# Performance work log

Hardware: AMD Instinct MI355X
Metric: run time of the kernel (lower is better)

## Reference

```python
import jax, jax.numpy as jnp
import numpy as np

DIM = 1280
HEADS = 16
HD = DIM // HEADS  # 80
NSEG = 8
LSEG = 1024
SEQ = NSEG * LSEG  # 8192


def _rotate_half(x):
    x1, x2 = jnp.split(x, 2, axis=-1)
    return jnp.concatenate([-x2, x1], axis=-1)


def setup_inputs() -> dict:
    key = jax.random.key(0)
    ks = jax.random.split(key, 6)
    hidden_states = jax.random.normal(ks[0], (SEQ, DIM), dtype=jnp.float32)
    # rotary embedding table: per-position angles over head_dim
    inv_freq = 1.0 / (10000.0 ** (np.arange(0, HD, 2, dtype=np.float32) / HD))
    pos = np.arange(SEQ, dtype=np.float32)
    freqs = np.outer(pos, inv_freq)                    # [SEQ, HD/2]
    emb = np.concatenate([freqs, freqs], axis=-1)      # [SEQ, HD]
    cos = jnp.asarray(np.cos(emb), dtype=jnp.float32)
    sin = jnp.asarray(np.sin(emb), dtype=jnp.float32)
    w_scale = 1.0 / np.sqrt(DIM)
    qkv_w = jax.random.normal(ks[1], (DIM, 3 * DIM), dtype=jnp.float32) * w_scale
    qkv_b = jax.random.normal(ks[2], (3 * DIM,), dtype=jnp.float32) * 0.02
    proj_w = jax.random.normal(ks[3], (DIM, DIM), dtype=jnp.float32) * w_scale
    proj_b = jax.random.normal(ks[4], (DIM,), dtype=jnp.float32) * 0.02
    cu_seqlens = jnp.arange(NSEG + 1, dtype=jnp.int32) * LSEG
    return {
        "hidden_states": hidden_states,
        "cos": cos,
        "sin": sin,
        "qkv_w": qkv_w,
        "qkv_b": qkv_b,
        "proj_w": proj_w,
        "proj_b": proj_b,
        "cu_seqlens": cu_seqlens,
    }


def reference(hidden_states, cos, sin, qkv_w, qkv_b, proj_w, proj_b, cu_seqlens):
    S, D = hidden_states.shape
    n_seg = cu_seqlens.shape[0] - 1          # static
    L = S // n_seg                            # equal-length packed segments
    # fused QKV projection: [S, 3D] -> q, k, v each [S, H, hd]
    qkv = hidden_states @ qkv_w + qkv_b
    q, k, v = (t.reshape(S, HEADS, HD) for t in jnp.split(qkv, 3, axis=-1))
    # RoPE (computed in fp32, as in apply_rotary_pos_emb_vision)
    c = cos.astype(jnp.float32)[:, None, :]   # [S, 1, hd]
    s = sin.astype(jnp.float32)[:, None, :]
    qf = q.astype(jnp.float32)
    kf = k.astype(jnp.float32)
    q = (qf * c + _rotate_half(qf) * s).astype(q.dtype)
    k = (kf * c + _rotate_half(kf) * s).astype(k.dtype)
    # block-diagonal varlen attention == independent attention per segment
    qs = q.reshape(n_seg, L, HEADS, HD)
    ks = k.reshape(n_seg, L, HEADS, HD)
    vs = v.reshape(n_seg, L, HEADS, HD)
    scale = HD ** -0.5
    scores = jnp.einsum("nqhd,nkhd->nhqk", qs, ks) * scale
    probs = jax.nn.softmax(scores.astype(jnp.float32), axis=-1).astype(qs.dtype)
    out = jnp.einsum("nhqk,nkhd->nqhd", probs, vs)     # [n, L, H, hd]
    out = out.reshape(S, D)
    return out @ proj_w + proj_b
```

## Files before the change

### kernel.cpp

```cpp
#include <hip/hip_runtime.h>

#define SEQ   8192
#define DIM   1280
#define HEADS 16
#define HD    80
#define LSEG  1024
#define QKVD  3840

typedef unsigned short USHORT;
typedef __attribute__((ext_vector_type(8))) short bf16x8;
typedef __attribute__((ext_vector_type(4))) float f32x4;
typedef __attribute__((ext_vector_type(4))) USHORT u16x4;
typedef __attribute__((ext_vector_type(4))) int i32x4;

#define CSF  0.16129832f
#define DTHR 71.554175f

__device__ __forceinline__ USHORT f2bf(float x) {
  unsigned u = __float_as_uint(x);
  u += 0x7fffu + ((u >> 16) & 1u);
  return (USHORT)(u >> 16);
}
__device__ __forceinline__ float bf2f(USHORT b) {
  return __uint_as_float(((unsigned)b) << 16);
}
__device__ __forceinline__ void gload16(const void* g, void* l) {
  __builtin_amdgcn_global_load_lds(
      (const __attribute__((address_space(1))) void*)g,
      (__attribute__((address_space(3))) void*)l, 16, 0, 0);
}
__device__ __forceinline__ unsigned cvtpk(float a, float b) {
  unsigned d;
  asm("v_cvt_pk_bf16_f32 %0, %1, %2" : "=v"(d) : "v"(a), "v"(b));
  return d;
}

__global__ __launch_bounds__(256) void prep1(
    const float* __restrict__ hs, USHORT* __restrict__ hsB,
    const float* __restrict__ qkv_w, USHORT* __restrict__ qkvwT,
    const float* __restrict__ proj_w, USHORT* __restrict__ pwT) {
  __shared__ float tb[32][33];
  const int bx = blockIdx.x;
  const int tid = threadIdx.x;
  if (bx < 10240) {
    const int i = bx * 256 + tid;
    const float4 v = reinterpret_cast<const float4*>(hs)[i];
    USHORT* o = hsB + (size_t)i * 4;
    o[0] = f2bf(v.x); o[1] = f2bf(v.y); o[2] = f2bf(v.z); o[3] = f2bf(v.w);
    return;
  }
  const float* W; USHORT* T; int K, N, n0, k0;
  if (bx < 15040) {
    const int b = bx - 10240;
    W = qkv_w; T = qkvwT; K = DIM; N = QKVD;
    n0 = (b % 120) * 32; k0 = (b / 120) * 32;
  } else {
    const int b = bx - 15040;
    W = proj_w; T = pwT; K = DIM; N = DIM;
    n0 = (b % 40) * 32; k0 = (b / 40) * 32;
  }
  const int c = tid & 31, r0 = tid >> 5;
  for (int r = r0; r < 32; r += 8) tb[r][c] = W[(size_t)(k0 + r) * N + n0 + c];
  __syncthreads();
  for (int r = r0; r < 32; r += 8)
    T[(size_t)(n0 + r) * K + k0 + c] = f2bf(tb[c][r]);
}

__global__ __launch_bounds__(256) void prep2(
    USHORT* __restrict__ qkv, const float* __restrict__ cosb,
    const float* __restrict__ sinb, USHORT* __restrict__ VtG,
    uint4* __restrict__ zb) {
  __shared__ USHORT tu[32][33];
  const int bx = blockIdx.x;
  const int tid = threadIdx.x;
  if (bx < 10240) {
    int idx = bx * 256 + tid;
    const int d4 = (idx % 10) * 4;
    int t = idx / 10;
    const int h = t % HEADS;
    t /= HEADS;
    const int qk = t & 1;
    const int s = t >> 1;
    USHORT* base = qkv + (size_t)s * QKVD + qk * DIM + h * HD;
    const u16x4 x1 = *(const u16x4*)&base[d4];
    const u16x4 x2 = *(const u16x4*)&base[d4 + 40];
    const f32x4 c1 = *(const f32x4*)&cosb[s * HD + d4];
    const f32x4 s1 = *(const f32x4*)&sinb[s * HD + d4];
    const f32x4 c2 = *(const f32x4*)&cosb[s * HD + d4 + 40];
    const f32x4 s2 = *(const f32x4*)&sinb[s * HD + d4 + 40];
    u16x4 o1, o2;
#pragma unroll
    for (int j = 0; j < 4; ++j) {
      const float a = bf2f(x1[j]), b = bf2f(x2[j]);
      o1[j] = f2bf(a * c1[j] - b * s1[j]);
      o2[j] = f2bf(b * c2[j] + a * s2[j]);
    }
    *(u16x4*)&base[d4] = o1;
    *(u16x4*)&base[d4 + 40] = o2;
    return;
  }
  if (bx < 20480) {
    const int b = bx - 10240;
    const int c0 = (b % 40) * 32, s0 = (b / 40) * 32;
    const int c = tid & 31, r0 = tid >> 5;
    for (int r = r0; r < 32; r += 8)
      tu[r][c] = qkv[(size_t)(s0 + r) * QKVD + 2 * DIM + c0 + c];
    __syncthreads();
    const int pc = (s0 & 32) | c;
    const int sc = (pc & 0x23) | ((pc & 0x10) >> 2) | ((pc & 0x0C) << 1);
    const size_t col = (size_t)(s0 & ~63) + sc;
    for (int r = r0; r < 32; r += 8)
      VtG[(size_t)(c0 + r) * SEQ + col] = tu[c][r];
    return;
  }
  if (tid < 64) zb[tid] = uint4{0u, 0u, 0u, 0u};
}

__global__ __launch_bounds__(512, 2) void mfma_gemm256(
    const USHORT* __restrict__ Ah, const USHORT* __restrict__ Bh,
    const float* __restrict__ bias, USHORT* __restrict__ Cout,
    int M, int N, int K, int lda) {
  extern __shared__ USHORT sm[];

  const int tid = threadIdx.x;
  const int l = tid & 63;
  const int w = tid >> 6;
  const int fr = l & 15;
  const int g = l >> 4;
  const int nrow = M >> 8;
  const int nwg = nrow * (N >> 8);
  const int orig = blockIdx.x;
  const int wg = (orig & 7) * (nwg >> 3) + (orig >> 3);
  const int row0 = (wg % nrow) << 8;
  const int col0 = (wg / nrow) << 8;
  const int wr = (w >> 2) << 7;
  const int wc = (w & 3) << 6;

  const f32x4 fz = {0.f, 0.f, 0.f, 0.f};
  f32x4 acc[8][4];
#pragma unroll
  for (int m = 0; m < 8; ++m)
#pragma unroll
    for (int n = 0; n < 4; ++n) acc[m][n] = fz;

  const int NT = K >> 6;

  const USHORT* asrc[4];
  const USHORT* bsrc[4];
#pragma unroll
  for (int i = 0; i < 4; ++i) {
    const int u = i * 512 + tid;
    const int row = u >> 3;
    const int c = (u & 7) ^ (row & 7);
    asrc[i] = Ah + (size_t)(row0 + row) * lda + c * 8;
    bsrc[i] = Bh + (size_t)(col0 + row) * K + c * 8;
  }
  auto stage = [&](int b) {
#pragma unroll
    for (int i = 0; i < 4; ++i) {
      USHORT* dst = sm + (i * 512 + (w << 6)) * 8 + b * 16384;
      gload16(asrc[i], dst);
      gload16(bsrc[i], dst + 32768);
    }
  };
  auto advance = [&]() {
#pragma unroll
    for (int i = 0; i < 4; ++i) { asrc[i] += 64; bsrc[i] += 64; }
  };

  const int fb = fr & 7;
  int aOff[2], bOff[2];
#pragma unroll
  for (int ks = 0; ks < 2; ++ks) {
    const int sl = (((ks << 2) + g) ^ fb) << 3;
    aOff[ks] = (wr + fr) * 64 + sl;
    bOff[ks] = 32768 + (wc + fr) * 64 + sl;
  }

  stage(0); advance();
  stage(1); advance();

  for (int t = 0; t < NT; ++t) {
    const int cur = t & 1;
    asm volatile("s_waitcnt vmcnt(8)" ::: "memory");
    __builtin_amdgcn_sched_barrier(0);
    __builtin_amdgcn_s_barrier();
    __builtin_amdgcn_sched_barrier(0);
    const int cb = cur << 14;
    bf16x8 ah[2][8], bh[2][4];
#pragma unroll
    for (int ks = 0; ks < 2; ++ks) {
#pragma unroll
      for (int m = 0; m < 8; ++m)
        ah[ks][m] = *(const bf16x8*)(sm + cb + aOff[ks] + m * 1024);
#pragma unroll
      for (int n = 0; n < 4; ++n)
        bh[ks][n] = *(const bf16x8*)(sm + cb + bOff[ks] + n * 1024);
    }
    asm volatile("s_waitcnt lgkmcnt(0)" ::: "memory");
    __builtin_amdgcn_sched_barrier(0);
    __builtin_amdgcn_s_barrier();
    __builtin_amdgcn_sched_barrier(0);
    stage(cur);
    if (t < NT - 3) advance();
    __builtin_amdgcn_sched_barrier(0);
    __builtin_amdgcn_s_setprio(1);
#pragma unroll
    for (int ks = 0; ks < 2; ++ks)
#pragma unroll
      for (int m = 0; m < 8; ++m)
#pragma unroll
        for (int n = 0; n < 4; ++n)
          acc[m][n] = __builtin_amdgcn_mfma_f32_16x16x32_bf16(
              ah[ks][m], bh[ks][n], acc[m][n], 0, 0, 0);
    __builtin_amdgcn_s_setprio(0);
  }

  asm volatile("s_waitcnt vmcnt(0)" ::: "memory");

  float bv[4];
#pragma unroll
  for (int n = 0; n < 4; ++n) bv[n] = bias[col0 + wc + n * 16 + fr];
#pragma unroll
  for (int m = 0; m < 8; ++m)
#pragma unroll
    for (int n = 0; n < 4; ++n)
#pragma unroll
      for (int r = 0; r < 4; ++r) {
        const float v = acc[m][n][r] + bv[n];
        const int row = row0 + wr + m * 16 + g * 4 + r;
        const int col = col0 + wc + n * 16 + fr;
        Cout[(size_t)row * N + col] = f2bf(v);
      }
}

template <int OUTBF>
__global__ __launch_bounds__(256) void mfma_gemm(
    const USHORT* __restrict__ Ah, const USHORT* __restrict__ Bh,
    const float* __restrict__ bias, void* __restrict__ Cout,
    int M, int N, int K, int lda) {
  __shared__ __align__(16) USHORT AhL[2][8192];
  __shared__ __align__(16) USHORT BhL[2][8192];

  const int tid = threadIdx.x;
  const int l = tid & 63;
  const int w = tid >> 6;
  const int nrow = M >> 7;
  const int nwg = nrow * (N >> 7);
  const int orig = blockIdx.x;
  const int wg = (orig & 7) * (nwg >> 3) + (orig >> 3);
  const int row0 = (wg % nrow) << 7;
  const int col0 = (wg / nrow) << 7;
  const int wr = (w >> 1) << 6;
  const int wc = (w & 1) << 6;

  const f32x4 fz = {0.f, 0.f, 0.f, 0.f};
  f32x4 acc[4][4];
#pragma unroll
  for (int m = 0; m < 4; ++m)
#pragma unroll
    for (int n = 0; n < 4; ++n) acc[m][n] = fz;

  const int fr = l & 15;
  const int g = l >> 4;
  const int NT = K >> 6;

  const USHORT* asrc[4];
  const USHORT* bsrc[4];
#pragma unroll
  for (int i = 0; i < 4; ++i) {
    const int u = (w * 4 + i) * 64 + l;
    const int row = u >> 3;
    const int c = (u & 7) ^ (row & 7);
    asrc[i] = Ah + (size_t)(row0 + row) * lda + c * 8;
    bsrc[i] = Bh + (size_t)(col0 + row) * K + c * 8;
  }
  auto stage = [&](int b) {
#pragma unroll
    for (int i = 0; i < 4; ++i) {
      gload16(asrc[i], &AhL[b][(w * 4 + i) * 512]);
      gload16(bsrc[i], &BhL[b][(w * 4 + i) * 512]);
    }
  };
  auto advance = [&]() {
#pragma unroll
    for (int i = 0; i < 4; ++i) { asrc[i] += 64; bsrc[i] += 64; }
  };

  const int fb = fr & 7;
  int aOff[2], bOff[2];
#pragma unroll
  for (int ks = 0; ks < 2; ++ks) {
    const int sl = (((ks << 2) + g) ^ fb) << 3;
    aOff[ks] = (wr + fr) * 64 + sl;
    bOff[ks] = (wc + fr) * 64 + sl;
  }
  const USHORT* AB = &AhL[0][0];
  const USHORT* BB = &BhL[0][0];

  stage(0); advance();
  stage(1); advance();

  for (int t = 0; t < NT; ++t) {
    const int cur = t & 1;
    asm volatile("s_waitcnt vmcnt(8)" ::: "memory");
    __builtin_amdgcn_sched_barrier(0);
    __builtin_amdgcn_s_barrier();
    __builtin_amdgcn_sched_barrier(0);
    const int cb = cur << 13;
    bf16x8 ah[2][4], bh[2][4];
#pragma unroll
    for (int ks = 0; ks < 2; ++ks)
#pragma unroll
      for (int m = 0; m < 4; ++m) {
        ah[ks][m] = *(const bf16x8*)(AB + cb + aOff[ks] + m * 1024);
        bh[ks][m] = *(const bf16x8*)(BB + cb + bOff[ks] + m * 1024);
      }
    asm volatile("s_waitcnt lgkmcnt(0)" ::: "memory");
    __builtin_amdgcn_sched_barrier(0);
    __builtin_amdgcn_s_barrier();
    __builtin_amdgcn_sched_barrier(0);
    stage(cur);
    if (t < NT - 3) advance();
    __builtin_amdgcn_sched_barrier(0);
    __builtin_amdgcn_s_setprio(1);
#pragma unroll
    for (int ks = 0; ks < 2; ++ks)
#pragma unroll
      for (int m = 0; m < 4; ++m)
#pragma unroll
        for (int n = 0; n < 4; ++n)
          acc[m][n] = __builtin_amdgcn_mfma_f32_16x16x32_bf16(
              ah[ks][m], bh[ks][n], acc[m][n], 0, 0, 0);
    __builtin_amdgcn_s_setprio(0);
  }

  asm volatile("s_waitcnt vmcnt(0)" ::: "memory");

  float bv[4];
#pragma unroll
  for (int n = 0; n < 4; ++n) bv[n] = bias[col0 + wc + n * 16 + fr];
#pragma unroll
  for (int m = 0; m < 4; ++m)
#pragma unroll
    for (int n = 0; n < 4; ++n)
#pragma unroll
      for (int r = 0; r < 4; ++r) {
        const float v = acc[m][n][r] + bv[n];
        const int row = row0 + wr + m * 16 + (l >> 4) * 4 + r;
        const int col = col0 + wc + n * 16 + fr;
        if (OUTBF)
          ((USHORT*)Cout)[(size_t)row * N + col] = f2bf(v);
        else
          ((float*)Cout)[(size_t)row * N + col] = v;
      }
}

__global__ __launch_bounds__(256, 3) void attn_mfma8(
    const USHORT* __restrict__ qkv, const USHORT* __restrict__ VtG,
    const USHORT* __restrict__ zbuf, USHORT* __restrict__ aoB) {
  const int h = blockIdx.y;
  const int bx = blockIdx.x;
  const int qb = (bx & 7) * 8 + (bx >> 3);
  const int s0 = qb * 128;
  const int k0g = (s0 / LSEG) * LSEG;
  const int tid = threadIdx.x;
  const int w = tid >> 6, l = tid & 63;
  const int g = l >> 4, fr = l & 15;
  const int q0 = s0 + w * 32;

  __shared__ __align__(16) USHORT Kl[2][64 * 128];
  __shared__ __align__(16) USHORT Vl[2][80 * 64];

  bf16x8 qb_frag[2][3];
#pragma unroll
  for (int nt2 = 0; nt2 < 2; ++nt2)
#pragma unroll
    for (int ks = 0; ks < 3; ++ks)
      qb_frag[nt2][ks] = *(const bf16x8*)
          &qkv[(size_t)(q0 + nt2 * 16 + fr) * QKVD + h * HD + ks * 32 + g * 8];

  const f32x4 fz = {0.f, 0.f, 0.f, 0.f};
  f32x4 oacc[2][5];
#pragma unroll
  for (int m = 0; m < 2; ++m)
#pragma unroll
    for (int n = 0; n < 5; ++n) oacc[m][n] = fz;
  float m_run[2] = {-3e38f, -3e38f};
  float l_run[2] = {0.f, 0.f};

  const int nV = (w < 2) ? 3 : 2;
  const int vbase = (w < 2) ? w * 3 : 6 + (w - 2) * 2;
  const USHORT* ksrc[4];
  int kstep[4];
#pragma unroll
  for (int i = 0; i < 4; ++i) {
    const int t = (w * 4 + i) * 64 + l;
    const int row = t >> 4, c = (t & 15) ^ (row & 7);
    if (c < 10) {
      ksrc[i] = qkv + (size_t)(k0g + row) * QKVD + DIM + h * HD + c * 8;
      kstep[i] = 64 * QKVD;
    } else {
      ksrc[i] = zbuf;
      kstep[i] = 0;
    }
  }
  const USHORT* vsrc[3] = {zbuf, zbuf, zbuf};
#pragma unroll
  for (int i = 0; i < 3; ++i)
    if (i < nV) {
      const int u = (vbase + i) * 64 + l;
      const int row = u >> 3, c = (u & 7) ^ (row & 7);
      vsrc[i] = VtG + (size_t)(h * HD + row) * SEQ + k0g + c * 8;
    }

  auto stageKV = [&](int kb, int b) {
#pragma unroll
    for (int i = 0; i < 4; ++i)
      gload16(ksrc[i] + (size_t)kb * kstep[i], &Kl[b][(w * 4 + i) * 512]);
#pragma unroll
    for (int i = 0; i < 3; ++i)
      if (i < nV)
        gload16(vsrc[i] + kb * 64, &Vl[b][(vbase + i) * 512]);
  };

  const int fb = fr & 7;
  int kOff[3], vOff[2];
#pragma unroll
  for (int ks = 0; ks < 3; ++ks)
    kOff[ks] = fr * 128 + ((((ks << 2) + g) ^ fb) << 3);
#pragma unroll
  for (int ks = 0; ks < 2; ++ks)
    vOff[ks] = fr * 64 + ((((ks << 2) + g) ^ fb) << 3);
  const USHORT* KB = &Kl[0][0];
  const USHORT* VB = &Vl[0][0];

  stageKV(0, 0);
  stageKV(1, 1);

  for (int kb = 0; kb < 16; ++kb) {
    const int cur = kb & 1;
    if (w < 2) {
      asm volatile("s_waitcnt vmcnt(7)" ::: "memory");
    } else {
      asm volatile("s_waitcnt vmcnt(6)" ::: "memory");
    }
    __builtin_amdgcn_sched_barrier(0);
    __builtin_amdgcn_s_barrier();
    __builtin_amdgcn_sched_barrier(0);
    const int kcb = cur << 13;
    const int vcb = cur * 5120;

    f32x4 sc[4][2];
#pragma unroll
    for (int m = 0; m < 4; ++m)
#pragma unroll
      for (int nt2 = 0; nt2 < 2; ++nt2) sc[m][nt2] = fz;
    __builtin_amdgcn_s_setprio(1);
#pragma unroll
    for (int ks = 0; ks < 3; ++ks)
#pragma unroll
      for (int m = 0; m < 4; ++m) {
        const bf16x8 kbf = *(const bf16x8*)(KB + kcb + kOff[ks] + m * 2048);
#pragma unroll
        for (int nt2 = 0; nt2 < 2; ++nt2)
          sc[m][nt2] = __builtin_amdgcn_mfma_f32_16x16x32_bf16(
              kbf, qb_frag[nt2][ks], sc[m][nt2], 0, 0, 0);
      }
    __builtin_amdgcn_s_setprio(0);

    float rmax[2];
#pragma unroll
    for (int nt2 = 0; nt2 < 2; ++nt2) {
      float mx = -3e38f;
#pragma unroll
      for (int m = 0; m < 4; ++m)
#pragma unroll
        for (int j = 0; j < 4; ++j) mx = fmaxf(mx, sc[m][nt2][j]);
      mx = fmaxf(mx, __shfl_xor(mx, 16));
      mx = fmaxf(mx, __shfl_xor(mx, 32));
      rmax[nt2] = mx;
    }
    const bool need =
        (rmax[0] > m_run[0] + DTHR) || (rmax[1] > m_run[1] + DTHR);
    if (__any(need)) {
      float fac[2];
#pragma unroll
      for (int nt2 = 0; nt2 < 2; ++nt2) {
        const float mn = fmaxf(m_run[nt2], rmax[nt2]);
        fac[nt2] = exp2f((m_run[nt2] - mn) * CSF);
        m_run[nt2] = mn;
        l_run[nt2] *= fac[nt2];
      }
#pragma unroll
      for (int mt2 = 0; mt2 < 2; ++mt2)
#pragma unroll
        for (int j = 0; j < 4; ++j) {
          const float fb2 = __shfl(fac[mt2], 20 * g + j);
#pragma unroll
          for (int nt = 0; nt < 5; ++nt) oacc[mt2][nt][j] *= fb2;
        }
    }
    unsigned pkr[2][4][2];
#pragma unroll
    for (int nt2 = 0; nt2 < 2; ++nt2) {
      const float mcs = m_run[nt2] * CSF;
      float ps = 0.f;
#pragma unroll
      for (int m = 0; m < 4; ++m) {
        float p[4];
#pragma unroll
        for (int j = 0; j < 4; ++j) {
          p[j] = exp2f(sc[m][nt2][j] * CSF - mcs);
          ps += p[j];
        }
        pkr[nt2][m][0] = cvtpk(p[0], p[1]);
        pkr[nt2][m][1] = cvtpk(p[2], p[3]);
      }
      ps += __shfl_xor(ps, 16);
      ps += __shfl_xor(ps, 32);
      l_run[nt2] += ps;
    }

#pragma unroll
    for (int ks = 0; ks < 2; ++ks) {
      union { bf16x8 v8; i32x4 i4; } pa[2];
#pragma unroll
      for (int mt2 = 0; mt2 < 2; ++mt2) {
        pa[mt2].i4[0] = (int)pkr[mt2][2 * ks][0];
        pa[mt2].i4[1] = (int)pkr[mt2][2 * ks][1];
        pa[mt2].i4[2] = (int)pkr[mt2][2 * ks + 1][0];
        pa[mt2].i4[3] = (int)pkr[mt2][2 * ks + 1][1];
      }
      __builtin_amdgcn_s_setprio(1);
#pragma unroll
      for (int nt = 0; nt < 5; ++nt) {
        const bf16x8 vb = *(const bf16x8*)(VB + vcb + vOff[ks] + nt * 1024);
#pragma unroll
        for (int mt2 = 0; mt2 < 2; ++mt2)
          oacc[mt2][nt] = __builtin_amdgcn_mfma_f32_16x16x32_bf16(
              pa[mt2].v8, vb, oacc[mt2][nt], 0, 0, 0);
      }
      __builtin_amdgcn_s_setprio(0);
    }

    __builtin_amdgcn_s_barrier();
    __builtin_amdgcn_sched_barrier(0);
    const int kn = (kb + 2 < 16) ? kb + 2 : kb;
    stageKV(kn, cur);
    __builtin_amdgcn_sched_barrier(0);
  }

  asm volatile("s_waitcnt vmcnt(0)" ::: "memory");

  float linv[2][4];
#pragma unroll
  for (int mt2 = 0; mt2 < 2; ++mt2)
#pragma unroll
    for (int j = 0; j < 4; ++j)
      linv[mt2][j] = 1.f / __shfl(l_run[mt2], 20 * g + j);
#pragma unroll
  for (int mt2 = 0; mt2 < 2; ++mt2)
#pragma unroll
    for (int nt = 0; nt < 5; ++nt)
#pragma unroll
      for (int j = 0; j < 4; ++j) {
        const int row = s0 + w * 32 + mt2 * 16 + g * 4 + j;
        const int col = h * HD + nt * 16 + fr;
        aoB[(size_t)row * QKVD + col] = f2bf(oacc[mt2][nt][j] * linv[mt2][j]);
      }
}

extern "C" void kernel_launch(void* const* d_in, const int* in_sizes, int n_in,
                              void* d_out, int out_size, void* d_ws,
                              size_t ws_size, hipStream_t stream) {
  const float* hs = (const float*)d_in[0];
  const float* cosb = (const float*)d_in[1];
  const float* sinb = (const float*)d_in[2];
  const float* qkv_w = (const float*)d_in[3];
  const float* qkv_b = (const float*)d_in[4];
  const float* proj_w = (const float*)d_in[5];
  const float* proj_b = (const float*)d_in[6];
  char* ws = (char*)d_ws;

  USHORT* qkvB  = (USHORT*)(ws);
  USHORT* hsB   = (USHORT*)(ws + 62914560u);
  USHORT* qkvwT = (USHORT*)(ws + 83886080u);
  USHORT* pwT   = (USHORT*)(ws + 93716480u);
  USHORT* VtG   = hsB;
  USHORT* zbuf  = qkvwT;
  USHORT* aoB   = qkvB + 2 * DIM;

  hipFuncSetAttribute((const void*)mfma_gemm256,
                      hipFuncAttributeMaxDynamicSharedMemorySize, 131072);

  prep1<<<16640, 256, 0, stream>>>(hs, hsB, qkv_w, qkvwT, proj_w, pwT);
  mfma_gemm256<<<(SEQ / 256) * (QKVD / 256), 512, 131072, stream>>>(
      hsB, qkvwT, qkv_b, qkvB, SEQ, QKVD, DIM, DIM);
  prep2<<<20481, 256, 0, stream>>>(qkvB, cosb, sinb, VtG, (uint4*)zbuf);
  attn_mfma8<<<dim3(SEQ / 128, HEADS), 256, 0, stream>>>(qkvB, VtG, zbuf, aoB);
  mfma_gemm<0><<<(SEQ / 128) * (DIM / 128), 256, 0, stream>>>(
      aoB, pwT, proj_b, d_out, SEQ, DIM, DIM, QKVD);
}
```

Baseline: 264.4 us.

## Fuse V transpose into QKV GEMM epilogue and overlap LDS reads with MFMA

The QKV GEMM epilogue writes V columns directly in the transposed, swizzled layout the attention kernel expects, using the output buffer as scratch, which removes the transpose pass from prep2. In both GEMMs and the attention kernel, LDS fragment loads are split per k-step with partial lgkmcnt waits so MFMAs on the first fragments start while later fragments are still loading. The cost is strided 8-byte epilogue stores for V and more fine-grained scheduling barriers.

```diff
diff --git a/kernel.cpp b/kernel.cpp
--- a/kernel.cpp
+++ b/kernel.cpp
@@ -34,6 +34,7 @@
   asm("v_cvt_pk_bf16_f32 %0, %1, %2" : "=v"(d) : "v"(a), "v"(b));
   return d;
 }
+#define SB() __builtin_amdgcn_sched_barrier(0)
 
 __global__ __launch_bounds__(256) void prep1(
     const float* __restrict__ hs, USHORT* __restrict__ hsB,
@@ -68,9 +69,7 @@
 
 __global__ __launch_bounds__(256) void prep2(
     USHORT* __restrict__ qkv, const float* __restrict__ cosb,
-    const float* __restrict__ sinb, USHORT* __restrict__ VtG,
-    uint4* __restrict__ zb) {
-  __shared__ USHORT tu[32][33];
+    const float* __restrict__ sinb, uint4* __restrict__ zb) {
   const int bx = blockIdx.x;
   const int tid = threadIdx.x;
   if (bx < 10240) {
@@ -99,27 +98,13 @@
     *(u16x4*)&base[d4 + 40] = o2;
     return;
   }
-  if (bx < 20480) {
-    const int b = bx - 10240;
-    const int c0 = (b % 40) * 32, s0 = (b / 40) * 32;
-    const int c = tid & 31, r0 = tid >> 5;
-    for (int r = r0; r < 32; r += 8)
-      tu[r][c] = qkv[(size_t)(s0 + r) * QKVD + 2 * DIM + c0 + c];
-    __syncthreads();
-    const int pc = (s0 & 32) | c;
-    const int sc = (pc & 0x23) | ((pc & 0x10) >> 2) | ((pc & 0x0C) << 1);
-    const size_t col = (size_t)(s0 & ~63) + sc;
-    for (int r = r0; r < 32; r += 8)
-      VtG[(size_t)(c0 + r) * SEQ + col] = tu[c][r];
-    return;
-  }
   if (tid < 64) zb[tid] = uint4{0u, 0u, 0u, 0u};
 }
 
 __global__ __launch_bounds__(512, 2) void mfma_gemm256(
     const USHORT* __restrict__ Ah, const USHORT* __restrict__ Bh,
     const float* __restrict__ bias, USHORT* __restrict__ Cout,
-    int M, int N, int K, int lda) {
+    USHORT* __restrict__ VtGo, int M, int N, int K, int lda) {
   extern __shared__ USHORT sm[];
 
   const int tid = threadIdx.x;
@@ -183,36 +168,50 @@
   for (int t = 0; t < NT; ++t) {
     const int cur = t & 1;
     asm volatile("s_waitcnt vmcnt(8)" ::: "memory");
-    __builtin_amdgcn_sched_barrier(0);
+    SB();
     __builtin_amdgcn_s_barrier();
-    __builtin_amdgcn_sched_barrier(0);
+    SB();
     const int cb = cur << 14;
     bf16x8 ah[2][8], bh[2][4];
 #pragma unroll
-    for (int ks = 0; ks < 2; ++ks) {
-#pragma unroll
-      for (int m = 0; m < 8; ++m)
-        ah[ks][m] = *(const bf16x8*)(sm + cb + aOff[ks] + m * 1024);
+    for (int m = 0; m < 8; ++m)
+      ah[0][m] = *(const bf16x8*)(sm + cb + aOff[0] + m * 1024);
+#pragma unroll
+    for (int n = 0; n < 4; ++n)
+      bh[0][n] = *(const bf16x8*)(sm + cb + bOff[0] + n * 1024);
+    SB();
+#pragma unroll
+    for (int m = 0; m < 8; ++m)
+      ah[1][m] = *(const bf16x8*)(sm + cb + aOff[1] + m * 1024);
+#pragma unroll
+    for (int n = 0; n < 4; ++n)
+      bh[1][n] = *(const bf16x8*)(sm + cb + bOff[1] + n * 1024);
+    SB();
+    asm volatile("s_waitcnt lgkmcnt(12)" ::: "memory");
+    SB();
+    __builtin_amdgcn_s_setprio(1);
+#pragma unroll
+    for (int m = 0; m < 8; ++m)
 #pragma unroll
       for (int n = 0; n < 4; ++n)
-        bh[ks][n] = *(const bf16x8*)(sm + cb + bOff[ks] + n * 1024);
-    }
+        acc[m][n] = __builtin_amdgcn_mfma_f32_16x16x32_bf16(
+            ah[0][m], bh[0][n], acc[m][n], 0, 0, 0);
+    __builtin_amdgcn_s_setprio(0);
+    SB();
     asm volatile("s_waitcnt lgkmcnt(0)" ::: "memory");
-    __builtin_amdgcn_sched_barrier(0);
+    SB();
     __builtin_amdgcn_s_barrier();
-    __builtin_amdgcn_sched_barrier(0);
+    SB();
     stage(cur);
     if (t < NT - 3) advance();
-    __builtin_amdgcn_sched_barrier(0);
-    __builtin_amdgcn_s_setprio(1);
-#pragma unroll
-    for (int ks = 0; ks < 2; ++ks)
-#pragma unroll
-      for (int m = 0; m < 8; ++m)
-#pragma unroll
-        for (int n = 0; n < 4; ++n)
-          acc[m][n] = __builtin_amdgcn_mfma_f32_16x16x32_bf16(
-              ah[ks][m], bh[ks][n], acc[m][n], 0, 0, 0);
+    SB();
+    __builtin_amdgcn_s_setprio(1);
+#pragma unroll
+    for (int m = 0; m < 8; ++m)
+#pragma unroll
+      for (int n = 0; n < 4; ++n)
+        acc[m][n] = __builtin_amdgcn_mfma_f32_16x16x32_bf16(
+            ah[1][m], bh[1][n], acc[m][n], 0, 0, 0);
     __builtin_amdgcn_s_setprio(0);
   }
 
@@ -224,20 +223,27 @@
 #pragma unroll
   for (int m = 0; m < 8; ++m)
 #pragma unroll
-    for (int n = 0; n < 4; ++n)
-#pragma unroll
-      for (int r = 0; r < 4; ++r) {
-        const float v = acc[m][n][r] + bv[n];
-        const int row = row0 + wr + m * 16 + g * 4 + r;
-        const int col = col0 + wc + n * 16 + fr;
-        Cout[(size_t)row * N + col] = f2bf(v);
+    for (int n = 0; n < 4; ++n) {
+      const int colb = col0 + wc + n * 16;
+      const int row = row0 + wr + m * 16 + g * 4;
+      if (colb >= 2 * DIM) {
+        u16x4 o;
+#pragma unroll
+        for (int r = 0; r < 4; ++r) o[r] = f2bf(acc[m][n][r] + bv[n]);
+        const int rl = row & 63;
+        const int sc = (rl & 0x23) | ((rl & 0x10) >> 2) | ((rl & 0x0C) << 1);
+        *(u16x4*)&VtGo[(size_t)(colb + fr - 2 * DIM) * SEQ + (row & ~63) + sc] = o;
+      } else {
+#pragma unroll
+        for (int r = 0; r < 4; ++r)
+          Cout[(size_t)(row + r) * N + colb + fr] = f2bf(acc[m][n][r] + bv[n]);
       }
-}
-
-template <int OUTBF>
+    }
+}
+
 __global__ __launch_bounds__(256) void mfma_gemm(
     const USHORT* __restrict__ Ah, const USHORT* __restrict__ Bh,
-    const float* __restrict__ bias, void* __restrict__ Cout,
+    const float* __restrict__ bias, float* __restrict__ Cout,
     int M, int N, int K, int lda) {
   __shared__ __align__(16) USHORT AhL[2][8192];
   __shared__ __align__(16) USHORT BhL[2][8192];
@@ -304,34 +310,48 @@
   for (int t = 0; t < NT; ++t) {
     const int cur = t & 1;
     asm volatile("s_waitcnt vmcnt(8)" ::: "memory");
-    __builtin_amdgcn_sched_barrier(0);
+    SB();
     __builtin_amdgcn_s_barrier();
-    __builtin_amdgcn_sched_barrier(0);
+    SB();
     const int cb = cur << 13;
     bf16x8 ah[2][4], bh[2][4];
 #pragma unroll
-    for (int ks = 0; ks < 2; ++ks)
-#pragma unroll
-      for (int m = 0; m < 4; ++m) {
-        ah[ks][m] = *(const bf16x8*)(AB + cb + aOff[ks] + m * 1024);
-        bh[ks][m] = *(const bf16x8*)(BB + cb + bOff[ks] + m * 1024);
-      }
+    for (int m = 0; m < 4; ++m) {
+      ah[0][m] = *(const bf16x8*)(AB + cb + aOff[0] + m * 1024);
+      bh[0][m] = *(const bf16x8*)(BB + cb + bOff[0] + m * 1024);
+    }
+    SB();
+#pragma unroll
+    for (int m = 0; m < 4; ++m) {
+      ah[1][m] = *(const bf16x8*)(AB + cb + aOff[1] + m * 1024);
+      bh[1][m] = *(const bf16x8*)(BB + cb + bOff[1] + m * 1024);
+    }
+    SB();
+    asm volatile("s_waitcnt lgkmcnt(8)" ::: "memory");
+    SB();
+    __builtin_amdgcn_s_setprio(1);
+#pragma unroll
+    for (int m = 0; m < 4; ++m)
+#pragma unroll
+      for (int n = 0; n < 4; ++n)
+        acc[m][n] = __builtin_amdgcn_mfma_f32_16x16x32_bf16(
+            ah[0][m], bh[0][n], acc[m][n], 0, 0, 0);
+    __builtin_amdgcn_s_setprio(0);
+    SB();
     asm volatile("s_waitcnt lgkmcnt(0)" ::: "memory");
-    __builtin_amdgcn_sched_barrier(0);
+    SB();
     __builtin_amdgcn_s_barrier();
-    __builtin_amdgcn_sched_barrier(0);
+    SB();
     stage(cur);
     if (t < NT - 3) advance();
-    __builtin_amdgcn_sched_barrier(0);
-    __builtin_amdgcn_s_setprio(1);
-#pragma unroll
-    for (int ks = 0; ks < 2; ++ks)
-#pragma unroll
-      for (int m = 0; m < 4; ++m)
-#pragma unroll
-        for (int n = 0; n < 4; ++n)
-          acc[m][n] = __builtin_amdgcn_mfma_f32_16x16x32_bf16(
-              ah[ks][m], bh[ks][n], acc[m][n], 0, 0, 0);
+    SB();
+    __builtin_amdgcn_s_setprio(1);
+#pragma unroll
+    for (int m = 0; m < 4; ++m)
+#pragma unroll
+      for (int n = 0; n < 4; ++n)
+        acc[m][n] = __builtin_amdgcn_mfma_f32_16x16x32_bf16(
+            ah[1][m], bh[1][n], acc[m][n], 0, 0, 0);
     __builtin_amdgcn_s_setprio(0);
   }
 
@@ -349,10 +369,7 @@
         const float v = acc[m][n][r] + bv[n];
         const int row = row0 + wr + m * 16 + (l >> 4) * 4 + r;
         const int col = col0 + wc + n * 16 + fr;
-        if (OUTBF)
-          ((USHORT*)Cout)[(size_t)row * N + col] = f2bf(v);
-        else
-          ((float*)Cout)[(size_t)row * N + col] = v;
+        Cout[(size_t)row * N + col] = v;
       }
 }
 
@@ -445,9 +462,9 @@
     } else {
       asm volatile("s_waitcnt vmcnt(6)" ::: "memory");
     }
-    __builtin_amdgcn_sched_barrier(0);
+    SB();
     __builtin_amdgcn_s_barrier();
-    __builtin_amdgcn_sched_barrier(0);
+    SB();
     const int kcb = cur << 13;
     const int vcb = cur * 5120;
 
@@ -456,18 +473,52 @@
     for (int m = 0; m < 4; ++m)
 #pragma unroll
       for (int nt2 = 0; nt2 < 2; ++nt2) sc[m][nt2] = fz;
-    __builtin_amdgcn_s_setprio(1);
-#pragma unroll
-    for (int ks = 0; ks < 3; ++ks)
-#pragma unroll
-      for (int m = 0; m < 4; ++m) {
-        const bf16x8 kbf = *(const bf16x8*)(KB + kcb + kOff[ks] + m * 2048);
-#pragma unroll
-        for (int nt2 = 0; nt2 < 2; ++nt2)
-          sc[m][nt2] = __builtin_amdgcn_mfma_f32_16x16x32_bf16(
-              kbf, qb_frag[nt2][ks], sc[m][nt2], 0, 0, 0);
-      }
-    __builtin_amdgcn_s_setprio(0);
+    bf16x8 kfa[4], kfb[4], kfc[4];
+#pragma unroll
+    for (int m = 0; m < 4; ++m)
+      kfa[m] = *(const bf16x8*)(KB + kcb + kOff[0] + m * 2048);
+    SB();
+#pragma unroll
+    for (int m = 0; m < 4; ++m)
+      kfb[m] = *(const bf16x8*)(KB + kcb + kOff[1] + m * 2048);
+    SB();
+    asm volatile("s_waitcnt lgkmcnt(4)" ::: "memory");
+    SB();
+    __builtin_amdgcn_s_setprio(1);
+#pragma unroll
+    for (int m = 0; m < 4; ++m)
+#pragma unroll
+      for (int nt2 = 0; nt2 < 2; ++nt2)
+        sc[m][nt2] = __builtin_amdgcn_mfma_f32_16x16x32_bf16(
+            kfa[m], qb_frag[nt2][0], sc[m][nt2], 0, 0, 0);
+    __builtin_amdgcn_s_setprio(0);
+    SB();
+#pragma unroll
+    for (int m = 0; m < 4; ++m)
+      kfc[m] = *(const bf16x8*)(KB + kcb + kOff[2] + m * 2048);
+    SB();
+    asm volatile("s_waitcnt lgkmcnt(4)" ::: "memory");
+    SB();
+    __builtin_amdgcn_s_setprio(1);
+#pragma unroll
+    for (int m = 0; m < 4; ++m)
+#pragma unroll
+      for (int nt2 = 0; nt2 < 2; ++nt2)
+        sc[m][nt2] = __builtin_amdgcn_mfma_f32_16x16x32_bf16(
+            kfb[m], qb_frag[nt2][1], sc[m][nt2], 0, 0, 0);
+    __builtin_amdgcn_s_setprio(0);
+    SB();
+    asm volatile("s_waitcnt lgkmcnt(0)" ::: "memory");
+    SB();
+    __builtin_amdgcn_s_setprio(1);
+#pragma unroll
+    for (int m = 0; m < 4; ++m)
+#pragma unroll
+      for (int nt2 = 0; nt2 < 2; ++nt2)
+        sc[m][nt2] = __builtin_amdgcn_mfma_f32_16x16x32_bf16(
+            kfc[m], qb_frag[nt2][2], sc[m][nt2], 0, 0, 0);
+    __builtin_amdgcn_s_setprio(0);
+    SB();
 
     float rmax[2];
 #pragma unroll
@@ -522,33 +573,54 @@
       l_run[nt2] += ps;
     }
 
-#pragma unroll
-    for (int ks = 0; ks < 2; ++ks) {
-      union { bf16x8 v8; i32x4 i4; } pa[2];
-#pragma unroll
-      for (int mt2 = 0; mt2 < 2; ++mt2) {
-        pa[mt2].i4[0] = (int)pkr[mt2][2 * ks][0];
-        pa[mt2].i4[1] = (int)pkr[mt2][2 * ks][1];
-        pa[mt2].i4[2] = (int)pkr[mt2][2 * ks + 1][0];
-        pa[mt2].i4[3] = (int)pkr[mt2][2 * ks + 1][1];
-      }
-      __builtin_amdgcn_s_setprio(1);
-#pragma unroll
-      for (int nt = 0; nt < 5; ++nt) {
-        const bf16x8 vb = *(const bf16x8*)(VB + vcb + vOff[ks] + nt * 1024);
-#pragma unroll
-        for (int mt2 = 0; mt2 < 2; ++mt2)
-          oacc[mt2][nt] = __builtin_amdgcn_mfma_f32_16x16x32_bf16(
-              pa[mt2].v8, vb, oacc[mt2][nt], 0, 0, 0);
-      }
-      __builtin_amdgcn_s_setprio(0);
-    }
+    bf16x8 vfa[5], vfb[5];
+#pragma unroll
+    for (int nt = 0; nt < 5; ++nt)
+      vfa[nt] = *(const bf16x8*)(VB + vcb + vOff[0] + nt * 1024);
+    SB();
+#pragma unroll
+    for (int nt = 0; nt < 5; ++nt)
+      vfb[nt] = *(const bf16x8*)(VB + vcb + vOff[1] + nt * 1024);
+    SB();
+    asm volatile("s_waitcnt lgkmcnt(5)" ::: "memory");
+    SB();
+    union { bf16x8 v8; i32x4 i4; } pa0[2], pa1[2];
+#pragma unroll
+    for (int mt2 = 0; mt2 < 2; ++mt2) {
+      pa0[mt2].i4[0] = (int)pkr[mt2][0][0];
+      pa0[mt2].i4[1] = (int)pkr[mt2][0][1];
+      pa0[mt2].i4[2] = (int)pkr[mt2][1][0];
+      pa0[mt2].i4[3] = (int)pkr[mt2][1][1];
+      pa1[mt2].i4[0] = (int)pkr[mt2][2][0];
+      pa1[mt2].i4[1] = (int)pkr[mt2][2][1];
+      pa1[mt2].i4[2] = (int)pkr[mt2][3][0];
+      pa1[mt2].i4[3] = (int)pkr[mt2][3][1];
+    }
+    __builtin_amdgcn_s_setprio(1);
+#pragma unroll
+    for (int nt = 0; nt < 5; ++nt)
+#pragma unroll
+      for (int mt2 = 0; mt2 < 2; ++mt2)
+        oacc[mt2][nt] = __builtin_amdgcn_mfma_f32_16x16x32_bf16(
+            pa0[mt2].v8, vfa[nt], oacc[mt2][nt], 0, 0, 0);
+    __builtin_amdgcn_s_setprio(0);
+    SB();
+    asm volatile("s_waitcnt lgkmcnt(0)" ::: "memory");
+    SB();
+    __builtin_amdgcn_s_setprio(1);
+#pragma unroll
+    for (int nt = 0; nt < 5; ++nt)
+#pragma unroll
+      for (int mt2 = 0; mt2 < 2; ++mt2)
+        oacc[mt2][nt] = __builtin_amdgcn_mfma_f32_16x16x32_bf16(
+            pa1[mt2].v8, vfb[nt], oacc[mt2][nt], 0, 0, 0);
+    __builtin_amdgcn_s_setprio(0);
 
     __builtin_amdgcn_s_barrier();
-    __builtin_amdgcn_sched_barrier(0);
+    SB();
     const int kn = (kb + 2 < 16) ? kb + 2 : kb;
     stageKV(kn, cur);
-    __builtin_amdgcn_sched_barrier(0);
+    SB();
   }
 
   asm volatile("s_waitcnt vmcnt(0)" ::: "memory");
@@ -587,7 +659,7 @@
   USHORT* hsB   = (USHORT*)(ws + 62914560u);
   USHORT* qkvwT = (USHORT*)(ws + 83886080u);
   USHORT* pwT   = (USHORT*)(ws + 93716480u);
-  USHORT* VtG   = hsB;
+  USHORT* VtG   = (USHORT*)d_out;
   USHORT* zbuf  = qkvwT;
   USHORT* aoB   = qkvB + 2 * DIM;
 
@@ -596,9 +668,9 @@
 
   prep1<<<16640, 256, 0, stream>>>(hs, hsB, qkv_w, qkvwT, proj_w, pwT);
   mfma_gemm256<<<(SEQ / 256) * (QKVD / 256), 512, 131072, stream>>>(
-      hsB, qkvwT, qkv_b, qkvB, SEQ, QKVD, DIM, DIM);
-  prep2<<<20481, 256, 0, stream>>>(qkvB, cosb, sinb, VtG, (uint4*)zbuf);
+      hsB, qkvwT, qkv_b, qkvB, VtG, SEQ, QKVD, DIM, DIM);
+  prep2<<<10241, 256, 0, stream>>>(qkvB, cosb, sinb, (uint4*)zbuf);
   attn_mfma8<<<dim3(SEQ / 128, HEADS), 256, 0, stream>>>(qkvB, VtG, zbuf, aoB);
-  mfma_gemm<0><<<(SEQ / 128) * (DIM / 128), 256, 0, stream>>>(
-      aoB, pwT, proj_b, d_out, SEQ, DIM, DIM, QKVD);
-}
+  mfma_gemm<<<(SEQ / 128) * (DIM / 128), 256, 0, stream>>>(
+      aoB, pwT, proj_b, (float*)d_out, SEQ, DIM, DIM, QKVD);
+}
```

Result: no change. 268.7 us (+1.6%).
